# Kernel tuning notes

Measured on AMD Instinct MI355X. Metric: run time of the kernel, lower is better.

## Reference

```python
import jax, jax.numpy as jnp
import numpy as np

FEAT_DIM = 64   # C
EMBED_DIM = 64  # E
NUM_HEADS = 4
B, K, H, W = 4, 8, 128, 128


def setup_inputs() -> dict:
    key = jax.random.key(0)
    ks = jax.random.split(key, 24)
    C, E = FEAT_DIM, EMBED_DIM

    def lin_w(k, out_d, in_d):
        return jax.random.normal(k, (out_d, in_d), jnp.float32) * (1.0 / np.sqrt(in_d))

    def lin_b(k, out_d):
        return jax.random.normal(k, (out_d,), jnp.float32) * 0.01

    return {
        "HF_star": jax.random.normal(ks[0], (B, C, H, W), jnp.float32),
        "HF_cands": jax.random.normal(ks[1], (B, K, C, H, W), jnp.float32),
        "Z_cands": jax.random.normal(ks[2], (B, K, C, H, W), jnp.float32),
        "q1_w": lin_w(ks[3], E, C + 2), "q1_b": lin_b(ks[4], E),
        "k1_w": lin_w(ks[5], E, C + 2), "k1_b": lin_b(ks[6], E),
        "v1_w": lin_w(ks[7], E, C), "v1_b": lin_b(ks[8], E),
        "q2_w": lin_w(ks[9], E, C + E + 2), "q2_b": lin_b(ks[10], E),
        "k2_w": lin_w(ks[11], E, C + E + 2), "k2_b": lin_b(ks[12], E),
        "v2_w": lin_w(ks[13], E, C + E), "v2_b": lin_b(ks[14], E),
        "in_proj_w": lin_w(ks[15], 3 * E, E), "in_proj_b": lin_b(ks[16], 3 * E),
        "out_w": lin_w(ks[17], E, E), "out_b": lin_b(ks[18], E),
    }


def _mha(q, k, v, in_proj_w, in_proj_b, out_w, out_b, num_heads):
    # Replicates torch nn.MultiheadAttention with query len 1 per pixel.
    # q: [BN, E], k/v: [BN, K, E]
    E = q.shape[-1]
    d = E // num_heads
    wq, wk, wv = jnp.split(in_proj_w, 3, axis=0)
    bq, bk, bv = jnp.split(in_proj_b, 3, axis=0)
    qh = (q @ wq.T + bq).reshape(-1, num_heads, d)                  # [BN,h,d]
    kh = (k @ wk.T + bk).reshape(k.shape[0], k.shape[1], num_heads, d)  # [BN,K,h,d]
    vh = (v @ wv.T + bv).reshape(v.shape[0], v.shape[1], num_heads, d)
    scale = 1.0 / np.sqrt(d).astype(np.float32)
    scores = jnp.einsum('bhd,bkhd->bhk', qh, kh) * scale            # [BN,h,K]
    attn = jax.nn.softmax(scores, axis=-1)
    out = jnp.einsum('bhk,bkhd->bhd', attn, vh).reshape(-1, E)      # [BN,E]
    return out @ out_w.T + out_b


def reference(HF_star, HF_cands, Z_cands,
              q1_w, q1_b, k1_w, k1_b, v1_w, v1_b,
              q2_w, q2_b, k2_w, k2_b, v2_w, v2_b,
              in_proj_w, in_proj_b, out_w, out_b):
    Bb, C, Hh, Ww = HF_star.shape
    Kk = HF_cands.shape[1]
    N = Hh * Ww
    E = out_w.shape[0]

    i = jnp.linspace(0.0, 1.0, Hh)
    j = jnp.linspace(0.0, 1.0, Ww)
    ig, jg = jnp.meshgrid(i, j, indexing='ij')
    coords = jnp.stack([ig, jg], axis=-1)                            # [H,W,2]

    Qpix = jnp.transpose(HF_star, (0, 2, 3, 1))                      # [B,H,W,C]
    Kc = jnp.transpose(HF_cands, (0, 1, 3, 4, 2))                    # [B,K,H,W,C]
    Vc = jnp.transpose(Z_cands, (0, 1, 3, 4, 2))                     # [B,K,H,W,C]
    coords_q = jnp.broadcast_to(coords, (Bb, Hh, Ww, 2))
    coords_k = jnp.broadcast_to(coords, (Bb, Kk, Hh, Ww, 2))

    # Stage 1 (note: key reshape [B,K,H,W,D] -> [B*N,K,D] matches torch reshape semantics)
    Q1 = jnp.concatenate([Qpix, coords_q], axis=-1).reshape(Bb * N, C + 2)
    K1 = jnp.concatenate([Kc, coords_k], axis=-1).reshape(Bb * N, Kk, C + 2)
    V1 = Vc.reshape(Bb * N, Kk, C)
    q = Q1 @ q1_w.T + q1_b
    k = K1 @ k1_w.T + k1_b
    v = V1 @ v1_w.T + v1_b
    z_star = _mha(q, k, v, in_proj_w, in_proj_b, out_w, out_b, NUM_HEADS)
    z_bhwe = z_star.reshape(Bb, Hh, Ww, E)                           # [B,H,W,E]
    z_k = jnp.broadcast_to(z_bhwe[:, None], (Bb, Kk, Hh, Ww, E))

    # Stage 2
    Q2 = jnp.concatenate([Qpix, z_bhwe, coords_q], axis=-1).reshape(Bb * N, C + E + 2)
    K2 = jnp.concatenate([Kc, z_k, coords_k], axis=-1).reshape(Bb * N, Kk, C + E + 2)
    V2 = jnp.concatenate([Vc, z_k], axis=-1).reshape(Bb * N, Kk, C + E)
    q = Q2 @ q2_w.T + q2_b
    k = K2 @ k2_w.T + k2_b
    v = V2 @ v2_w.T + v2_b
    z_hat = _mha(q, k, v, in_proj_w, in_proj_b, out_w, out_b, NUM_HEADS)
    return jnp.transpose(z_hat.reshape(Bb, Hh, Ww, E), (0, 3, 1, 2))  # [B,E,H,W]
```

## Files before the change

### kernel.cpp

```cpp
#include <hip/hip_runtime.h>
#include <math.h>

#define HWp 16384
#define CH 64
#define KC 8
#define WSTRIDE 136

typedef __attribute__((ext_vector_type(8))) short bf16x8;
typedef __attribute__((ext_vector_type(4))) float f32x4;

#define MFMA(a, b, c) __builtin_amdgcn_mfma_f32_16x16x32_bf16(a, b, c, 0, 0, 0)

__device__ __forceinline__ short f2bf(float f) {
  unsigned u = __float_as_uint(f);
  u += 0x7FFFu + ((u >> 16) & 1u);
  return (short)(u >> 16);
}
__device__ __forceinline__ float bf2f(short s) {
  return __uint_as_float(((unsigned)(unsigned short)s) << 16);
}

__device__ __forceinline__ bf16x8 ldB(const short* __restrict__ W, int nrow, int c0) {
  return *(const bf16x8*)(W + nrow * WSTRIDE + c0);
}
__device__ __forceinline__ bf16x8 ldA_g(const float* __restrict__ base, int c0, int row) {
  bf16x8 f;
#pragma unroll
  for (int j = 0; j < 8; ++j) f[j] = f2bf(base[(size_t)(c0 + j) * HWp + row]);
  return f;
}
__device__ __forceinline__ bf16x8 ldA_z(const short* __restrict__ zrow, int c0) {
  return *(const bf16x8*)(zrow + c0);
}

__global__ void setup_weights(const float* __restrict__ q1w, const float* __restrict__ q1b,
                              const float* __restrict__ k1w, const float* __restrict__ k1b,
                              const float* __restrict__ v1w, const float* __restrict__ v1b,
                              const float* __restrict__ q2w, const float* __restrict__ q2b,
                              const float* __restrict__ k2w, const float* __restrict__ k2b,
                              const float* __restrict__ v2w, const float* __restrict__ v2b,
                              const float* __restrict__ ipw, const float* __restrict__ ipb,
                              const float* __restrict__ ow, short* __restrict__ Wt,
                              float* __restrict__ Bc) {
  int id = blockIdx.y;
  int idx = blockIdx.x * 256 + threadIdx.x;
  if (id == 6) {
    if (idx < 4096) {
      int e = idx >> 6, d = idx & 63;
      Wt[(6 * 64 + e) * WSTRIDE + d] = f2bf(ow[e * 64 + d]);
    }
    return;
  }
  const float* lw; const float* lb; int K, off;
  switch (id) {
    case 0:  lw = q1w; lb = q1b; K = 66;  off = 0;   break;
    case 1:  lw = k1w; lb = k1b; K = 66;  off = 64;  break;
    case 2:  lw = v1w; lb = v1b; K = 64;  off = 128; break;
    case 3:  lw = q2w; lb = q2b; K = 130; off = 0;   break;
    case 4:  lw = k2w; lb = k2b; K = 130; off = 64;  break;
    default: lw = v2w; lb = v2b; K = 128; off = 128; break;
  }
  if (idx < K * 64) {
    int c = idx >> 6, e = idx & 63;
    float s = 0.f;
    for (int f = 0; f < 64; ++f) s += ipw[(off + e) * 64 + f] * lw[f * K + c];
    Wt[(id * 64 + e) * WSTRIDE + c] = f2bf(s);
  } else if (idx < K * 64 + 64) {
    int e = idx - K * 64;
    float s = ipb[off + e];
    for (int f = 0; f < 64; ++f) s += ipw[(off + e) * 64 + f] * lb[f];
    Bc[id * 64 + e] = s;
  }
}

__global__ __launch_bounds__(256) void stage1(const float* __restrict__ HFs,
                                              const float* __restrict__ HFc,
                                              const float* __restrict__ Zc,
                                              const short* __restrict__ Wt,
                                              const float* __restrict__ Bc,
                                              const float* __restrict__ outb,
                                              short* __restrict__ zb) {
  const int t = threadIdx.x;
  const int wv = t >> 6, l = t & 63;
  const int tile = blockIdx.x;
  const int b = tile >> 11;
  const int p0 = (tile & 2047) << 3;
  const int m0 = p0 << 3;
  const int k0 = m0 >> 14;
  const int poff = m0 & (HWp - 1);

  __shared__ float KV[64 * 77];
  __shared__ float QH[8 * 68];
  __shared__ float AO[8 * 68];
  __shared__ float ATT[256];

  const int am = l & 15, kg = l >> 4, n = l & 15;
  const int row0 = wv * 16;

  const short* Wq = Wt + 0 * 64 * WSTRIDE;
  const short* Wk = Wt + 1 * 64 * WSTRIDE;
  const short* Wv = Wt + 2 * 64 * WSTRIDE;
  const short* Wo = Wt + 6 * 64 * WSTRIDE;
  const float* BQ = Bc + 0 * 64;
  const float* BK = Bc + 1 * 64;
  const float* BV = Bc + 2 * 64;

  const float* baseKc = HFc + ((size_t)(b * KC + k0) * CH) * HWp + poff;
  const float* baseZc = Zc + ((size_t)(b * KC + k0) * CH) * HWp + poff;
  const float* baseQ = HFs + (size_t)b * CH * HWp;
  const float inv127 = 1.f / 127.f;

  f32x4 kacc[4];
#pragma unroll
  for (int ct = 0; ct < 4; ++ct) {
    int col = ct * 16 + n;
    float bk = BK[col];
    float wi = bf2f(Wk[col * WSTRIDE + 64]);
    float wj = bf2f(Wk[col * WSTRIDE + 65]);
#pragma unroll
    for (int r = 0; r < 4; ++r) {
      int pp = poff + row0 + kg * 4 + r;
      kacc[ct][r] = bk + (float)(pp >> 7) * inv127 * wi + (float)(pp & 127) * inv127 * wj;
    }
  }
  f32x4 qacc;
  {
    int colq = wv * 16 + n;
    float bq = BQ[colq];
    float wi = bf2f(Wq[colq * WSTRIDE + 64]);
    float wj = bf2f(Wq[colq * WSTRIDE + 65]);
#pragma unroll
    for (int r = 0; r < 4; ++r) {
      int p = p0 + ((kg * 4 + r) & 7);
      qacc[r] = bq + (float)(p >> 7) * inv127 * wi + (float)(p & 127) * inv127 * wj;
    }
  }
#pragma unroll
  for (int ks = 0; ks < 2; ++ks) {
    int c0 = ks * 32 + kg * 8;
    bf16x8 a = ldA_g(baseKc, c0, row0 + am);
#pragma unroll
    for (int ct = 0; ct < 4; ++ct) kacc[ct] = MFMA(a, ldB(Wk, ct * 16 + n, c0), kacc[ct]);
    bf16x8 aq = ldA_g(baseQ, c0, p0 + (am & 7));
    qacc = MFMA(aq, ldB(Wq, wv * 16 + n, c0), qacc);
  }
#pragma unroll
  for (int ct = 0; ct < 4; ++ct)
#pragma unroll
    for (int r = 0; r < 4; ++r)
      KV[(row0 + kg * 4 + r) * 77 + ct * 16 + n] = kacc[ct][r];
#pragma unroll
  for (int r = 0; r < 4; ++r) {
    int m = kg * 4 + r;
    if (m < 8) QH[m * 68 + wv * 16 + n] = qacc[r];
  }
  __syncthreads();

  {
    int p = t >> 5, k = t & 7, h = (t >> 3) & 3;
    const float* qrow = &QH[p * 68 + h * 16];
    const float* krow = &KV[(p * 8 + k) * 77 + h * 16];
    float s = 0.f;
#pragma unroll
    for (int d = 0; d < 16; ++d) s += qrow[d] * krow[d];
    s *= 0.25f;
    float mx = s;
    mx = fmaxf(mx, __shfl_xor(mx, 1));
    mx = fmaxf(mx, __shfl_xor(mx, 2));
    mx = fmaxf(mx, __shfl_xor(mx, 4));
    float e = __expf(s - mx);
    float sum = e;
    sum += __shfl_xor(sum, 1);
    sum += __shfl_xor(sum, 2);
    sum += __shfl_xor(sum, 4);
    ATT[t] = e / sum;
  }
  __syncthreads();

  f32x4 vacc[4];
#pragma unroll
  for (int ct = 0; ct < 4; ++ct) {
    float bv = BV[ct * 16 + n];
#pragma unroll
    for (int r = 0; r < 4; ++r) vacc[ct][r] = bv;
  }
#pragma unroll
  for (int ks = 0; ks < 2; ++ks) {
    int c0 = ks * 32 + kg * 8;
    bf16x8 a = ldA_g(baseZc, c0, row0 + am);
#pragma unroll
    for (int ct = 0; ct < 4; ++ct) vacc[ct] = MFMA(a, ldB(Wv, ct * 16 + n, c0), vacc[ct]);
  }
#pragma unroll
  for (int ct = 0; ct < 4; ++ct)
#pragma unroll
    for (int r = 0; r < 4; ++r)
      KV[(row0 + kg * 4 + r) * 77 + ct * 16 + n] = vacc[ct][r];
  __syncthreads();

  {
    int p = t >> 5, dp = t & 7, h = (t >> 3) & 3;
    int d0 = h * 16 + dp * 2;
    float o0 = 0.f, o1 = 0.f;
#pragma unroll
    for (int k = 0; k < 8; ++k) {
      float a = ATT[(t & ~7) + k];
      const float* vrow = &KV[(p * 8 + k) * 77 + d0];
      o0 += a * vrow[0];
      o1 += a * vrow[1];
    }
    AO[p * 68 + d0] = o0;
    AO[p * 68 + d0 + 1] = o1;
  }
  __syncthreads();

  {
    int colo = wv * 16 + n;
    f32x4 oacc;
    float bo = outb[colo];
#pragma unroll
    for (int r = 0; r < 4; ++r) oacc[r] = bo;
#pragma unroll
    for (int ks = 0; ks < 2; ++ks) {
      int c0 = ks * 32 + kg * 8;
      bf16x8 a;
#pragma unroll
      for (int j = 0; j < 8; ++j) a[j] = f2bf(AO[(am & 7) * 68 + c0 + j]);
      oacc = MFMA(a, ldB(Wo, colo, c0), oacc);
    }
#pragma unroll
    for (int r = 0; r < 4; ++r) {
      int m = kg * 4 + r;
      if (m < 8) zb[((size_t)(b * HWp + p0 + m)) * 64 + colo] = f2bf(oacc[r]);
    }
  }
}

__global__ __launch_bounds__(256) void stage2(const float* __restrict__ HFs,
                                              const float* __restrict__ HFc,
                                              const float* __restrict__ Zc,
                                              const short* __restrict__ Wt,
                                              const float* __restrict__ Bc,
                                              const float* __restrict__ outb,
                                              const short* __restrict__ zb,
                                              float* __restrict__ out) {
  const int t = threadIdx.x;
  const int wv = t >> 6, l = t & 63;
  const int tile = blockIdx.x;
  const int b = tile >> 11;
  const int p0 = (tile & 2047) << 3;
  const int m0 = p0 << 3;
  const int k0 = m0 >> 14;
  const int poff = m0 & (HWp - 1);

  __shared__ float KV[64 * 77];
  __shared__ float QH[8 * 68];
  __shared__ float AO[8 * 68];
  __shared__ float ATT[256];

  const int am = l & 15, kg = l >> 4, n = l & 15;
  const int row0 = wv * 16;

  const short* Wq = Wt + 3 * 64 * WSTRIDE;
  const short* Wk = Wt + 4 * 64 * WSTRIDE;
  const short* Wv = Wt + 5 * 64 * WSTRIDE;
  const short* Wo = Wt + 6 * 64 * WSTRIDE;
  const float* BQ = Bc + 3 * 64;
  const float* BK = Bc + 4 * 64;
  const float* BV = Bc + 5 * 64;

  const float* baseKc = HFc + ((size_t)(b * KC + k0) * CH) * HWp + poff;
  const float* baseZc = Zc + ((size_t)(b * KC + k0) * CH) * HWp + poff;
  const float* baseQ = HFs + (size_t)b * CH * HWp;
  const short* zK = zb + ((size_t)(b * HWp + poff + row0 + am)) * 64;
  const short* zQ = zb + ((size_t)(b * HWp + p0 + (am & 7))) * 64;
  const float inv127 = 1.f / 127.f;

  f32x4 kacc[4];
#pragma unroll
  for (int ct = 0; ct < 4; ++ct) {
    int col = ct * 16 + n;
    float bk = BK[col];
    float wi = bf2f(Wk[col * WSTRIDE + 128]);
    float wj = bf2f(Wk[col * WSTRIDE + 129]);
#pragma unroll
    for (int r = 0; r < 4; ++r) {
      int pp = poff + row0 + kg * 4 + r;
      kacc[ct][r] = bk + (float)(pp >> 7) * inv127 * wi + (float)(pp & 127) * inv127 * wj;
    }
  }
  f32x4 qacc;
  {
    int colq = wv * 16 + n;
    float bq = BQ[colq];
    float wi = bf2f(Wq[colq * WSTRIDE + 128]);
    float wj = bf2f(Wq[colq * WSTRIDE + 129]);
#pragma unroll
    for (int r = 0; r < 4; ++r) {
      int p = p0 + ((kg * 4 + r) & 7);
      qacc[r] = bq + (float)(p >> 7) * inv127 * wi + (float)(p & 127) * inv127 * wj;
    }
  }
#pragma unroll
  for (int ks = 0; ks < 4; ++ks) {
    int c0 = ks * 32 + kg * 8;
    bf16x8 a = (ks < 2) ? ldA_g(baseKc, c0, row0 + am) : ldA_z(zK, c0 - 64);
#pragma unroll
    for (int ct = 0; ct < 4; ++ct) kacc[ct] = MFMA(a, ldB(Wk, ct * 16 + n, c0), kacc[ct]);
    bf16x8 aq = (ks < 2) ? ldA_g(baseQ, c0, p0 + (am & 7)) : ldA_z(zQ, c0 - 64);
    qacc = MFMA(aq, ldB(Wq, wv * 16 + n, c0), qacc);
  }
#pragma unroll
  for (int ct = 0; ct < 4; ++ct)
#pragma unroll
    for (int r = 0; r < 4; ++r)
      KV[(row0 + kg * 4 + r) * 77 + ct * 16 + n] = kacc[ct][r];
#pragma unroll
  for (int r = 0; r < 4; ++r) {
    int m = kg * 4 + r;
    if (m < 8) QH[m * 68 + wv * 16 + n] = qacc[r];
  }
  __syncthreads();

  {
    int p = t >> 5, k = t & 7, h = (t >> 3) & 3;
    const float* qrow = &QH[p * 68 + h * 16];
    const float* krow = &KV[(p * 8 + k) * 77 + h * 16];
    float s = 0.f;
#pragma unroll
    for (int d = 0; d < 16; ++d) s += qrow[d] * krow[d];
    s *= 0.25f;
    float mx = s;
    mx = fmaxf(mx, __shfl_xor(mx, 1));
    mx = fmaxf(mx, __shfl_xor(mx, 2));
    mx = fmaxf(mx, __shfl_xor(mx, 4));
    float e = __expf(s - mx);
    float sum = e;
    sum += __shfl_xor(sum, 1);
    sum += __shfl_xor(sum, 2);
    sum += __shfl_xor(sum, 4);
    ATT[t] = e / sum;
  }
  __syncthreads();

  f32x4 vacc[4];
#pragma unroll
  for (int ct = 0; ct < 4; ++ct) {
    float bv = BV[ct * 16 + n];
#pragma unroll
    for (int r = 0; r < 4; ++r) vacc[ct][r] = bv;
  }
#pragma unroll
  for (int ks = 0; ks < 4; ++ks) {
    int c0 = ks * 32 + kg * 8;
    bf16x8 a = (ks < 2) ? ldA_g(baseZc, c0, row0 + am) : ldA_z(zK, c0 - 64);
#pragma unroll
    for (int ct = 0; ct < 4; ++ct) vacc[ct] = MFMA(a, ldB(Wv, ct * 16 + n, c0), vacc[ct]);
  }
#pragma unroll
  for (int ct = 0; ct < 4; ++ct)
#pragma unroll
    for (int r = 0; r < 4; ++r)
      KV[(row0 + kg * 4 + r) * 77 + ct * 16 + n] = vacc[ct][r];
  __syncthreads();

  {
    int p = t >> 5, dp = t & 7, h = (t >> 3) & 3;
    int d0 = h * 16 + dp * 2;
    float o0 = 0.f, o1 = 0.f;
#pragma unroll
    for (int k = 0; k < 8; ++k) {
      float a = ATT[(t & ~7) + k];
      const float* vrow = &KV[(p * 8 + k) * 77 + d0];
      o0 += a * vrow[0];
      o1 += a * vrow[1];
    }
    AO[p * 68 + d0] = o0;
    AO[p * 68 + d0 + 1] = o1;
  }
  __syncthreads();

  {
    int colo = wv * 16 + n;
    f32x4 oacc;
    float bo = outb[colo];
#pragma unroll
    for (int r = 0; r < 4; ++r) oacc[r] = bo;
#pragma unroll
    for (int ks = 0; ks < 2; ++ks) {
      int c0 = ks * 32 + kg * 8;
      bf16x8 a;
#pragma unroll
      for (int j = 0; j < 8; ++j) a[j] = f2bf(AO[(am & 7) * 68 + c0 + j]);
      oacc = MFMA(a, ldB(Wo, colo, c0), oacc);
    }
#pragma unroll
    for (int r = 0; r < 4; ++r) {
      int m = kg * 4 + r;
      if (m < 8) out[((size_t)(b * 64 + colo)) * HWp + p0 + m] = oacc[r];
    }
  }
}

extern "C" void kernel_launch(void* const* d_in, const int* in_sizes, int n_in,
                              void* d_out, int out_size, void* d_ws, size_t ws_size,
                              hipStream_t stream) {
  const float* HFs = (const float*)d_in[0];
  const float* HFc = (const float*)d_in[1];
  const float* Zc = (const float*)d_in[2];
  const float* q1w = (const float*)d_in[3];  const float* q1b = (const float*)d_in[4];
  const float* k1w = (const float*)d_in[5];  const float* k1b = (const float*)d_in[6];
  const float* v1w = (const float*)d_in[7];  const float* v1b = (const float*)d_in[8];
  const float* q2w = (const float*)d_in[9];  const float* q2b = (const float*)d_in[10];
  const float* k2w = (const float*)d_in[11]; const float* k2b = (const float*)d_in[12];
  const float* v2w = (const float*)d_in[13]; const float* v2b = (const float*)d_in[14];
  const float* ipw = (const float*)d_in[15]; const float* ipb = (const float*)d_in[16];
  const float* ow = (const float*)d_in[17];  const float* ob = (const float*)d_in[18];

  short* Wt = (short*)d_ws;
  float* Bc = (float*)((char*)d_ws + 121856);
  short* zb = (short*)((char*)d_ws + 131072);
  float* out = (float*)d_out;

  dim3 gsetup(33, 7);
  setup_weights<<<gsetup, 256, 0, stream>>>(q1w, q1b, k1w, k1b, v1w, v1b,
                                            q2w, q2b, k2w, k2b, v2w, v2b,
                                            ipw, ipb, ow, Wt, Bc);
  stage1<<<8192, 256, 0, stream>>>(HFs, HFc, Zc, Wt, Bc, ob, zb);
  stage2<<<8192, 256, 0, stream>>>(HFs, HFc, Zc, Wt, Bc, ob, zb, out);
}
```

Baseline: 542.7 us.

## Stage channel-major activation tiles into swizzled LDS with vectorized loads

Replaces per-lane scalar strided global loads (8 channels at HWp stride each) for the K, V and Q MFMA operands with a cooperative up-front staging step. Each thread issues float4 loads along the pixel dimension, converts to bf16, and writes into XOR-swizzled shared tiles. MFMA A-operands are then read as 16-byte LDS vectors. This aims to coalesce global traffic and cut redundant uncoalesced loads, at the cost of roughly 17KB extra LDS per block (lower occupancy) and an added barrier. V loads are now issued early, before attention, which also overlaps them.

```diff
diff --git a/kernel.cpp b/kernel.cpp
--- a/kernel.cpp
+++ b/kernel.cpp
@@ -23,14 +23,44 @@
 __device__ __forceinline__ bf16x8 ldB(const short* __restrict__ W, int nrow, int c0) {
   return *(const bf16x8*)(W + nrow * WSTRIDE + c0);
 }
-__device__ __forceinline__ bf16x8 ldA_g(const float* __restrict__ base, int c0, int row) {
-  bf16x8 f;
-#pragma unroll
-  for (int j = 0; j < 8; ++j) f[j] = f2bf(base[(size_t)(c0 + j) * HWp + row]);
-  return f;
-}
 __device__ __forceinline__ bf16x8 ldA_z(const short* __restrict__ zrow, int c0) {
   return *(const bf16x8*)(zrow + c0);
+}
+
+__device__ __forceinline__ bf16x8 ldT(const short* tile, int p, int c0) {
+  return *(const bf16x8*)(tile + p * 64 + ((((c0 >> 3) ^ p) & 7) << 3));
+}
+
+__device__ __forceinline__ void stage_tile(short* dst, const float* __restrict__ src, int t) {
+  const int ch = (t >> 3) << 1;
+  const int pg = (t & 7) << 3;
+  const float* r0 = src + (size_t)ch * HWp + pg;
+  const float* r1 = r0 + HWp;
+  f32x4 a0 = *(const f32x4*)r0;
+  f32x4 a1 = *(const f32x4*)(r0 + 4);
+  f32x4 b0 = *(const f32x4*)r1;
+  f32x4 b1 = *(const f32x4*)(r1 + 4);
+  const int cb = (ch >> 3) & 7;
+  const int cs = ch & 7;
+#pragma unroll
+  for (int j = 0; j < 8; ++j) {
+    float fa = (j < 4) ? a0[j & 3] : a1[j & 3];
+    float fb = (j < 4) ? b0[j & 3] : b1[j & 3];
+    unsigned dw = (unsigned)(unsigned short)f2bf(fa) |
+                  ((unsigned)(unsigned short)f2bf(fb) << 16);
+    *(unsigned*)(dst + (pg + j) * 64 + ((cb ^ j) << 3) + cs) = dw;
+  }
+}
+
+__device__ __forceinline__ void stage_q(short* dst, const float* __restrict__ src, int t) {
+  const int c = t >> 2;
+  const int p2 = (t & 3) << 1;
+  float x0 = src[(size_t)c * HWp + p2];
+  float x1 = src[(size_t)c * HWp + p2 + 1];
+  const int cb = (c >> 3) & 7;
+  const int cs = c & 7;
+  dst[p2 * 64 + ((cb ^ (p2 & 7)) << 3) + cs] = f2bf(x0);
+  dst[(p2 + 1) * 64 + ((cb ^ ((p2 + 1) & 7)) << 3) + cs] = f2bf(x1);
 }
 
 __global__ void setup_weights(const float* __restrict__ q1w, const float* __restrict__ q1b,
@@ -93,6 +123,9 @@
   __shared__ float QH[8 * 68];
   __shared__ float AO[8 * 68];
   __shared__ float ATT[256];
+  __shared__ __align__(16) short KT[64 * 64];
+  __shared__ __align__(16) short VT[64 * 64];
+  __shared__ __align__(16) short QT[8 * 64];
 
   const int am = l & 15, kg = l >> 4, n = l & 15;
   const int row0 = wv * 16;
@@ -110,6 +143,10 @@
   const float* baseQ = HFs + (size_t)b * CH * HWp;
   const float inv127 = 1.f / 127.f;
 
+  stage_tile(KT, baseKc, t);
+  stage_tile(VT, baseZc, t);
+  stage_q(QT, baseQ + p0, t);
+
   f32x4 kacc[4];
 #pragma unroll
   for (int ct = 0; ct < 4; ++ct) {
@@ -135,13 +172,14 @@
       qacc[r] = bq + (float)(p >> 7) * inv127 * wi + (float)(p & 127) * inv127 * wj;
     }
   }
+  __syncthreads();
 #pragma unroll
   for (int ks = 0; ks < 2; ++ks) {
     int c0 = ks * 32 + kg * 8;
-    bf16x8 a = ldA_g(baseKc, c0, row0 + am);
+    bf16x8 a = ldT(KT, row0 + am, c0);
 #pragma unroll
     for (int ct = 0; ct < 4; ++ct) kacc[ct] = MFMA(a, ldB(Wk, ct * 16 + n, c0), kacc[ct]);
-    bf16x8 aq = ldA_g(baseQ, c0, p0 + (am & 7));
+    bf16x8 aq = ldT(QT, am & 7, c0);
     qacc = MFMA(aq, ldB(Wq, wv * 16 + n, c0), qacc);
   }
 #pragma unroll
@@ -187,7 +225,7 @@
 #pragma unroll
   for (int ks = 0; ks < 2; ++ks) {
     int c0 = ks * 32 + kg * 8;
-    bf16x8 a = ldA_g(baseZc, c0, row0 + am);
+    bf16x8 a = ldT(VT, row0 + am, c0);
 #pragma unroll
     for (int ct = 0; ct < 4; ++ct) vacc[ct] = MFMA(a, ldB(Wv, ct * 16 + n, c0), vacc[ct]);
   }
@@ -257,6 +295,9 @@
   __shared__ float QH[8 * 68];
   __shared__ float AO[8 * 68];
   __shared__ float ATT[256];
+  __shared__ __align__(16) short KT[64 * 64];
+  __shared__ __align__(16) short VT[64 * 64];
+  __shared__ __align__(16) short QT[8 * 64];
 
   const int am = l & 15, kg = l >> 4, n = l & 15;
   const int row0 = wv * 16;
@@ -276,6 +317,10 @@
   const short* zQ = zb + ((size_t)(b * HWp + p0 + (am & 7))) * 64;
   const float inv127 = 1.f / 127.f;
 
+  stage_tile(KT, baseKc, t);
+  stage_tile(VT, baseZc, t);
+  stage_q(QT, baseQ + p0, t);
+
   f32x4 kacc[4];
 #pragma unroll
   for (int ct = 0; ct < 4; ++ct) {
@@ -301,13 +346,14 @@
       qacc[r] = bq + (float)(p >> 7) * inv127 * wi + (float)(p & 127) * inv127 * wj;
     }
   }
+  __syncthreads();
 #pragma unroll
   for (int ks = 0; ks < 4; ++ks) {
     int c0 = ks * 32 + kg * 8;
-    bf16x8 a = (ks < 2) ? ldA_g(baseKc, c0, row0 + am) : ldA_z(zK, c0 - 64);
+    bf16x8 a = (ks < 2) ? ldT(KT, row0 + am, c0) : ldA_z(zK, c0 - 64);
 #pragma unroll
     for (int ct = 0; ct < 4; ++ct) kacc[ct] = MFMA(a, ldB(Wk, ct * 16 + n, c0), kacc[ct]);
-    bf16x8 aq = (ks < 2) ? ldA_g(baseQ, c0, p0 + (am & 7)) : ldA_z(zQ, c0 - 64);
+    bf16x8 aq = (ks < 2) ? ldT(QT, am & 7, c0) : ldA_z(zQ, c0 - 64);
     qacc = MFMA(aq, ldB(Wq, wv * 16 + n, c0), qacc);
   }
 #pragma unroll
@@ -353,7 +399,7 @@
 #pragma unroll
   for (int ks = 0; ks < 4; ++ks) {
     int c0 = ks * 32 + kg * 8;
-    bf16x8 a = (ks < 2) ? ldA_g(baseZc, c0, row0 + am) : ldA_z(zK, c0 - 64);
+    bf16x8 a = (ks < 2) ? ldT(VT, row0 + am, c0) : ldA_z(zK, c0 - 64);
 #pragma unroll
     for (int ct = 0; ct < 4; ++ct) vacc[ct] = MFMA(a, ldB(Wv, ct * 16 + n, c0), vacc[ct]);
   }
```

After: 495.7 us. 8.7% less time.

## Stage coalesced bf16 input tiles in swizzled LDS with register prefetch across 4 tiles

Applied to the files above, without the earlier changes.

Each block now processes four 8-pixel tiles instead of one, cutting the grid from 8192 to 2048 blocks. Input candidate and query features are loaded with vectorized float4 coalesced reads into registers, converted to bf16, and written into XOR-swizzled LDS tiles. The next tile's loads are double-buffered in registers so global latency overlaps compute. This replaces the old strided scalar per-element global gathers, at the cost of more LDS and registers, which may lower occupancy.

```diff
diff --git a/kernel.cpp b/kernel.cpp
--- a/kernel.cpp
+++ b/kernel.cpp
@@ -5,6 +5,7 @@
 #define CH 64
 #define KC 8
 #define WSTRIDE 136
+#define NT 4
 
 typedef __attribute__((ext_vector_type(8))) short bf16x8;
 typedef __attribute__((ext_vector_type(4))) float f32x4;
@@ -23,14 +24,56 @@
 __device__ __forceinline__ bf16x8 ldB(const short* __restrict__ W, int nrow, int c0) {
   return *(const bf16x8*)(W + nrow * WSTRIDE + c0);
 }
-__device__ __forceinline__ bf16x8 ldA_g(const float* __restrict__ base, int c0, int row) {
-  bf16x8 f;
-#pragma unroll
-  for (int j = 0; j < 8; ++j) f[j] = f2bf(base[(size_t)(c0 + j) * HWp + row]);
-  return f;
-}
-__device__ __forceinline__ bf16x8 ldA_z(const short* __restrict__ zrow, int c0) {
-  return *(const bf16x8*)(zrow + c0);
+
+__device__ __forceinline__ bf16x8 ldT(const short* tile, int p, int c0) {
+  return *(const bf16x8*)(tile + p * 64 + ((((c0 >> 3) ^ p) & 7) << 3));
+}
+
+struct Stage {
+  f32x4 k[4];
+  f32x4 v[4];
+  float q0, q1;
+};
+
+__device__ __forceinline__ void ld_rows(f32x4 v[4], const float* __restrict__ src, int t) {
+  const int chg = t >> 4, pxg = t & 15;
+  const float* r = src + (size_t)(chg << 2) * HWp + (pxg << 2);
+#pragma unroll
+  for (int i = 0; i < 4; ++i) v[i] = *(const f32x4*)(r + (size_t)i * HWp);
+}
+
+__device__ __forceinline__ void ld_stage(Stage& s, const float* __restrict__ bK,
+                                         const float* __restrict__ bV,
+                                         const float* __restrict__ bQ, int t) {
+  ld_rows(s.k, bK, t);
+  ld_rows(s.v, bV, t);
+  const int c = t >> 2, p2 = (t & 3) << 1;
+  s.q0 = bQ[(size_t)c * HWp + p2];
+  s.q1 = bQ[(size_t)c * HWp + p2 + 1];
+}
+
+__device__ __forceinline__ void wr_rows(short* dst, const f32x4 v[4], int t) {
+  const int chg = t >> 4, pxg = t & 15;
+  const int ch4 = chg << 2;
+  const int cb = (ch4 >> 3) & 7;
+  const int sub = (ch4 & 7) >> 1;
+#pragma unroll
+  for (int jj = 0; jj < 4; ++jj) {
+    int p = (pxg << 2) + jj;
+    unsigned d0 = (unsigned)(unsigned short)f2bf(v[0][jj]) |
+                  ((unsigned)(unsigned short)f2bf(v[1][jj]) << 16);
+    unsigned d1 = (unsigned)(unsigned short)f2bf(v[2][jj]) |
+                  ((unsigned)(unsigned short)f2bf(v[3][jj]) << 16);
+    unsigned* q = (unsigned*)dst + p * 32 + (((cb ^ (p & 7)) & 7) << 2) + sub;
+    *(uint2*)q = make_uint2(d0, d1);
+  }
+}
+
+__device__ __forceinline__ void wr_q(short* dst, float q0, float q1, int t) {
+  const int c = t >> 2, p2 = (t & 3) << 1;
+  const int cb = (c >> 3) & 7, cs = c & 7;
+  dst[p2 * 64 + (((cb ^ p2) & 7) << 3) + cs] = f2bf(q0);
+  dst[(p2 + 1) * 64 + (((cb ^ (p2 + 1)) & 7) << 3) + cs] = f2bf(q1);
 }
 
 __global__ void setup_weights(const float* __restrict__ q1w, const float* __restrict__ q1b,
@@ -82,17 +125,21 @@
                                               short* __restrict__ zb) {
   const int t = threadIdx.x;
   const int wv = t >> 6, l = t & 63;
-  const int tile = blockIdx.x;
-  const int b = tile >> 11;
-  const int p0 = (tile & 2047) << 3;
-  const int m0 = p0 << 3;
-  const int k0 = m0 >> 14;
-  const int poff = m0 & (HWp - 1);
+  const int bid = blockIdx.x;
+  const int b = bid >> 9;
+  const int pt0 = (bid & 511) << 2;
+  const int p0b = pt0 << 3;
+  const int m0b = p0b << 3;
+  const int k0 = m0b >> 14;
+  const int poffb = m0b & (HWp - 1);
 
   __shared__ float KV[64 * 77];
   __shared__ float QH[8 * 68];
   __shared__ float AO[8 * 68];
   __shared__ float ATT[256];
+  __shared__ __align__(16) short KT[64 * 64];
+  __shared__ __align__(16) short VT[64 * 64];
+  __shared__ __align__(16) short QT[8 * 64];
 
   const int am = l & 15, kg = l >> 4, n = l & 15;
   const int row0 = wv * 16;
@@ -105,134 +152,159 @@
   const float* BK = Bc + 1 * 64;
   const float* BV = Bc + 2 * 64;
 
-  const float* baseKc = HFc + ((size_t)(b * KC + k0) * CH) * HWp + poff;
-  const float* baseZc = Zc + ((size_t)(b * KC + k0) * CH) * HWp + poff;
+  const float* baseKc = HFc + ((size_t)(b * KC + k0) * CH) * HWp + poffb;
+  const float* baseZc = Zc + ((size_t)(b * KC + k0) * CH) * HWp + poffb;
   const float* baseQ = HFs + (size_t)b * CH * HWp;
   const float inv127 = 1.f / 127.f;
 
-  f32x4 kacc[4];
-#pragma unroll
-  for (int ct = 0; ct < 4; ++ct) {
-    int col = ct * 16 + n;
-    float bk = BK[col];
-    float wi = bf2f(Wk[col * WSTRIDE + 64]);
-    float wj = bf2f(Wk[col * WSTRIDE + 65]);
-#pragma unroll
-    for (int r = 0; r < 4; ++r) {
-      int pp = poff + row0 + kg * 4 + r;
-      kacc[ct][r] = bk + (float)(pp >> 7) * inv127 * wi + (float)(pp & 127) * inv127 * wj;
-    }
-  }
-  f32x4 qacc;
-  {
-    int colq = wv * 16 + n;
-    float bq = BQ[colq];
-    float wi = bf2f(Wq[colq * WSTRIDE + 64]);
-    float wj = bf2f(Wq[colq * WSTRIDE + 65]);
-#pragma unroll
-    for (int r = 0; r < 4; ++r) {
-      int p = p0 + ((kg * 4 + r) & 7);
-      qacc[r] = bq + (float)(p >> 7) * inv127 * wi + (float)(p & 127) * inv127 * wj;
-    }
-  }
-#pragma unroll
-  for (int ks = 0; ks < 2; ++ks) {
-    int c0 = ks * 32 + kg * 8;
-    bf16x8 a = ldA_g(baseKc, c0, row0 + am);
-#pragma unroll
-    for (int ct = 0; ct < 4; ++ct) kacc[ct] = MFMA(a, ldB(Wk, ct * 16 + n, c0), kacc[ct]);
-    bf16x8 aq = ldA_g(baseQ, c0, p0 + (am & 7));
-    qacc = MFMA(aq, ldB(Wq, wv * 16 + n, c0), qacc);
-  }
-#pragma unroll
-  for (int ct = 0; ct < 4; ++ct)
-#pragma unroll
-    for (int r = 0; r < 4; ++r)
-      KV[(row0 + kg * 4 + r) * 77 + ct * 16 + n] = kacc[ct][r];
-#pragma unroll
-  for (int r = 0; r < 4; ++r) {
-    int m = kg * 4 + r;
-    if (m < 8) QH[m * 68 + wv * 16 + n] = qacc[r];
-  }
+  Stage st[2];
+  ld_stage(st[0], baseKc, baseZc, baseQ + p0b, t);
+  ld_stage(st[1], baseKc + 64, baseZc + 64, baseQ + p0b + 8, t);
+  wr_rows(KT, st[0].k, t);
+  wr_rows(VT, st[0].v, t);
+  wr_q(QT, st[0].q0, st[0].q1, t);
   __syncthreads();
 
-  {
-    int p = t >> 5, k = t & 7, h = (t >> 3) & 3;
-    const float* qrow = &QH[p * 68 + h * 16];
-    const float* krow = &KV[(p * 8 + k) * 77 + h * 16];
-    float s = 0.f;
-#pragma unroll
-    for (int d = 0; d < 16; ++d) s += qrow[d] * krow[d];
-    s *= 0.25f;
-    float mx = s;
-    mx = fmaxf(mx, __shfl_xor(mx, 1));
-    mx = fmaxf(mx, __shfl_xor(mx, 2));
-    mx = fmaxf(mx, __shfl_xor(mx, 4));
-    float e = __expf(s - mx);
-    float sum = e;
-    sum += __shfl_xor(sum, 1);
-    sum += __shfl_xor(sum, 2);
-    sum += __shfl_xor(sum, 4);
-    ATT[t] = e / sum;
-  }
-  __syncthreads();
-
-  f32x4 vacc[4];
-#pragma unroll
-  for (int ct = 0; ct < 4; ++ct) {
-    float bv = BV[ct * 16 + n];
-#pragma unroll
-    for (int r = 0; r < 4; ++r) vacc[ct][r] = bv;
-  }
-#pragma unroll
-  for (int ks = 0; ks < 2; ++ks) {
-    int c0 = ks * 32 + kg * 8;
-    bf16x8 a = ldA_g(baseZc, c0, row0 + am);
-#pragma unroll
-    for (int ct = 0; ct < 4; ++ct) vacc[ct] = MFMA(a, ldB(Wv, ct * 16 + n, c0), vacc[ct]);
-  }
-#pragma unroll
-  for (int ct = 0; ct < 4; ++ct)
-#pragma unroll
-    for (int r = 0; r < 4; ++r)
-      KV[(row0 + kg * 4 + r) * 77 + ct * 16 + n] = vacc[ct][r];
-  __syncthreads();
-
-  {
-    int p = t >> 5, dp = t & 7, h = (t >> 3) & 3;
-    int d0 = h * 16 + dp * 2;
-    float o0 = 0.f, o1 = 0.f;
-#pragma unroll
-    for (int k = 0; k < 8; ++k) {
-      float a = ATT[(t & ~7) + k];
-      const float* vrow = &KV[(p * 8 + k) * 77 + d0];
-      o0 += a * vrow[0];
-      o1 += a * vrow[1];
-    }
-    AO[p * 68 + d0] = o0;
-    AO[p * 68 + d0 + 1] = o1;
-  }
-  __syncthreads();
-
-  {
-    int colo = wv * 16 + n;
-    f32x4 oacc;
-    float bo = outb[colo];
-#pragma unroll
-    for (int r = 0; r < 4; ++r) oacc[r] = bo;
+#pragma unroll
+  for (int j = 0; j < NT; ++j) {
+    const int p0 = p0b + j * 8;
+    const int poff = poffb + j * 64;
+
+    f32x4 kacc[4];
+#pragma unroll
+    for (int ct = 0; ct < 4; ++ct) {
+      int col = ct * 16 + n;
+      float bk = BK[col];
+      float wi = bf2f(Wk[col * WSTRIDE + 64]);
+      float wj = bf2f(Wk[col * WSTRIDE + 65]);
+#pragma unroll
+      for (int r = 0; r < 4; ++r) {
+        int pp = poff + row0 + kg * 4 + r;
+        kacc[ct][r] = bk + (float)(pp >> 7) * inv127 * wi + (float)(pp & 127) * inv127 * wj;
+      }
+    }
+    f32x4 qacc;
+    {
+      int colq = wv * 16 + n;
+      float bq = BQ[colq];
+      float wi = bf2f(Wq[colq * WSTRIDE + 64]);
+      float wj = bf2f(Wq[colq * WSTRIDE + 65]);
+#pragma unroll
+      for (int r = 0; r < 4; ++r) {
+        int p = p0 + ((kg * 4 + r) & 7);
+        qacc[r] = bq + (float)(p >> 7) * inv127 * wi + (float)(p & 127) * inv127 * wj;
+      }
+    }
 #pragma unroll
     for (int ks = 0; ks < 2; ++ks) {
       int c0 = ks * 32 + kg * 8;
-      bf16x8 a;
-#pragma unroll
-      for (int j = 0; j < 8; ++j) a[j] = f2bf(AO[(am & 7) * 68 + c0 + j]);
-      oacc = MFMA(a, ldB(Wo, colo, c0), oacc);
-    }
+      bf16x8 a = ldT(KT, row0 + am, c0);
+#pragma unroll
+      for (int ct = 0; ct < 4; ++ct) kacc[ct] = MFMA(a, ldB(Wk, ct * 16 + n, c0), kacc[ct]);
+      bf16x8 aq = ldT(QT, am & 7, c0);
+      qacc = MFMA(aq, ldB(Wq, wv * 16 + n, c0), qacc);
+    }
+#pragma unroll
+    for (int ct = 0; ct < 4; ++ct)
+#pragma unroll
+      for (int r = 0; r < 4; ++r)
+        KV[(row0 + kg * 4 + r) * 77 + ct * 16 + n] = kacc[ct][r];
 #pragma unroll
     for (int r = 0; r < 4; ++r) {
       int m = kg * 4 + r;
-      if (m < 8) zb[((size_t)(b * HWp + p0 + m)) * 64 + colo] = f2bf(oacc[r]);
-    }
+      if (m < 8) QH[m * 68 + wv * 16 + n] = qacc[r];
+    }
+    __syncthreads();
+
+    {
+      int p = t >> 5, k = t & 7, h = (t >> 3) & 3;
+      const float* qrow = &QH[p * 68 + h * 16];
+      const float* krow = &KV[(p * 8 + k) * 77 + h * 16];
+      float s = 0.f;
+#pragma unroll
+      for (int d = 0; d < 16; ++d) s += qrow[d] * krow[d];
+      s *= 0.25f;
+      float mx = s;
+      mx = fmaxf(mx, __shfl_xor(mx, 1));
+      mx = fmaxf(mx, __shfl_xor(mx, 2));
+      mx = fmaxf(mx, __shfl_xor(mx, 4));
+      float e = __expf(s - mx);
+      float sum = e;
+      sum += __shfl_xor(sum, 1);
+      sum += __shfl_xor(sum, 2);
+      sum += __shfl_xor(sum, 4);
+      ATT[t] = e / sum;
+    }
+    __syncthreads();
+
+    f32x4 vacc[4];
+#pragma unroll
+    for (int ct = 0; ct < 4; ++ct) {
+      float bv = BV[ct * 16 + n];
+#pragma unroll
+      for (int r = 0; r < 4; ++r) vacc[ct][r] = bv;
+    }
+#pragma unroll
+    for (int ks = 0; ks < 2; ++ks) {
+      int c0 = ks * 32 + kg * 8;
+      bf16x8 a = ldT(VT, row0 + am, c0);
+#pragma unroll
+      for (int ct = 0; ct < 4; ++ct) vacc[ct] = MFMA(a, ldB(Wv, ct * 16 + n, c0), vacc[ct]);
+    }
+#pragma unroll
+    for (int ct = 0; ct < 4; ++ct)
+#pragma unroll
+      for (int r = 0; r < 4; ++r)
+        KV[(row0 + kg * 4 + r) * 77 + ct * 16 + n] = vacc[ct][r];
+    __syncthreads();
+
+    {
+      int p = t >> 5, dp = t & 7, h = (t >> 3) & 3;
+      int d0 = h * 16 + dp * 2;
+      float o0 = 0.f, o1 = 0.f;
+#pragma unroll
+      for (int k = 0; k < 8; ++k) {
+        float a = ATT[(t & ~7) + k];
+        const float* vrow = &KV[(p * 8 + k) * 77 + d0];
+        o0 += a * vrow[0];
+        o1 += a * vrow[1];
+      }
+      AO[p * 68 + d0] = o0;
+      AO[p * 68 + d0 + 1] = o1;
+    }
+    __syncthreads();
+
+    {
+      int colo = wv * 16 + n;
+      f32x4 oacc;
+      float bo = outb[colo];
+#pragma unroll
+      for (int r = 0; r < 4; ++r) oacc[r] = bo;
+#pragma unroll
+      for (int ks = 0; ks < 2; ++ks) {
+        int c0 = ks * 32 + kg * 8;
+        bf16x8 a;
+#pragma unroll
+        for (int q = 0; q < 8; ++q) a[q] = f2bf(AO[(am & 7) * 68 + c0 + q]);
+        oacc = MFMA(a, ldB(Wo, colo, c0), oacc);
+      }
+#pragma unroll
+      for (int r = 0; r < 4; ++r) {
+        int m = kg * 4 + r;
+        if (m < 8) zb[((size_t)(b * HWp + p0 + m)) * 64 + colo] = f2bf(oacc[r]);
+      }
+    }
+
+    if (j < NT - 1) {
+      Stage& nx = st[(j + 1) & 1];
+      wr_rows(KT, nx.k, t);
+      wr_rows(VT, nx.v, t);
+      wr_q(QT, nx.q0, nx.q1, t);
+      if (j < NT - 2)
+        ld_stage(st[j & 1], baseKc + (j + 2) * 64, baseZc + (j + 2) * 64,
+                 baseQ + p0b + (j + 2) * 8, t);
+    }
+    __syncthreads();
   }
 }
 
@@ -246,17 +318,21 @@
                                               float* __restrict__ out) {
   const int t = threadIdx.x;
   const int wv = t >> 6, l = t & 63;
-  const int tile = blockIdx.x;
-  const int b = tile >> 11;
-  const int p0 = (tile & 2047) << 3;
-  const int m0 = p0 << 3;
-  const int k0 = m0 >> 14;
-  const int poff = m0 & (HWp - 1);
+  const int bid = blockIdx.x;
+  const int b = bid >> 9;
+  const int pt0 = (bid & 511) << 2;
+  const int p0b = pt0 << 3;
+  const int m0b = p0b << 3;
+  const int k0 = m0b >> 14;
+  const int poffb = m0b & (HWp - 1);
 
   __shared__ float KV[64 * 77];
   __shared__ float QH[8 * 68];
   __shared__ float AO[8 * 68];
   __shared__ float ATT[256];
+  __shared__ __align__(16) short KT[64 * 64];
+  __shared__ __align__(16) short VT[64 * 64];
+  __shared__ __align__(16) short QT[8 * 64];
 
   const int am = l & 15, kg = l >> 4, n = l & 15;
   const int row0 = wv * 16;
@@ -269,136 +345,166 @@
   const float* BK = Bc + 4 * 64;
   const float* BV = Bc + 5 * 64;
 
-  const float* baseKc = HFc + ((size_t)(b * KC + k0) * CH) * HWp + poff;
-  const float* baseZc = Zc + ((size_t)(b * KC + k0) * CH) * HWp + poff;
+  const float* baseKc = HFc + ((size_t)(b * KC + k0) * CH) * HWp + poffb;
+  const float* baseZc = Zc + ((size_t)(b * KC + k0) * CH) * HWp + poffb;
   const float* baseQ = HFs + (size_t)b * CH * HWp;
-  const short* zK = zb + ((size_t)(b * HWp + poff + row0 + am)) * 64;
-  const short* zQ = zb + ((size_t)(b * HWp + p0 + (am & 7))) * 64;
   const float inv127 = 1.f / 127.f;
 
-  f32x4 kacc[4];
-#pragma unroll
-  for (int ct = 0; ct < 4; ++ct) {
-    int col = ct * 16 + n;
-    float bk = BK[col];
-    float wi = bf2f(Wk[col * WSTRIDE + 128]);
-    float wj = bf2f(Wk[col * WSTRIDE + 129]);
-#pragma unroll
-    for (int r = 0; r < 4; ++r) {
-      int pp = poff + row0 + kg * 4 + r;
-      kacc[ct][r] = bk + (float)(pp >> 7) * inv127 * wi + (float)(pp & 127) * inv127 * wj;
-    }
-  }
-  f32x4 qacc;
-  {
-    int colq = wv * 16 + n;
-    float bq = BQ[colq];
-    float wi = bf2f(Wq[colq * WSTRIDE + 128]);
-    float wj = bf2f(Wq[colq * WSTRIDE + 129]);
-#pragma unroll
-    for (int r = 0; r < 4; ++r) {
-      int p = p0 + ((kg * 4 + r) & 7);
-      qacc[r] = bq + (float)(p >> 7) * inv127 * wi + (float)(p & 127) * inv127 * wj;
-    }
-  }
-#pragma unroll
-  for (int ks = 0; ks < 4; ++ks) {
-    int c0 = ks * 32 + kg * 8;
-    bf16x8 a = (ks < 2) ? ldA_g(baseKc, c0, row0 + am) : ldA_z(zK, c0 - 64);
-#pragma unroll
-    for (int ct = 0; ct < 4; ++ct) kacc[ct] = MFMA(a, ldB(Wk, ct * 16 + n, c0), kacc[ct]);
-    bf16x8 aq = (ks < 2) ? ldA_g(baseQ, c0, p0 + (am & 7)) : ldA_z(zQ, c0 - 64);
-    qacc = MFMA(aq, ldB(Wq, wv * 16 + n, c0), qacc);
-  }
-#pragma unroll
-  for (int ct = 0; ct < 4; ++ct)
-#pragma unroll
-    for (int r = 0; r < 4; ++r)
-      KV[(row0 + kg * 4 + r) * 77 + ct * 16 + n] = kacc[ct][r];
-#pragma unroll
-  for (int r = 0; r < 4; ++r) {
-    int m = kg * 4 + r;
-    if (m < 8) QH[m * 68 + wv * 16 + n] = qacc[r];
-  }
+  Stage st[2];
+  ld_stage(st[0], baseKc, baseZc, baseQ + p0b, t);
+  ld_stage(st[1], baseKc + 64, baseZc + 64, baseQ + p0b + 8, t);
+  wr_rows(KT, st[0].k, t);
+  wr_rows(VT, st[0].v, t);
+  wr_q(QT, st[0].q0, st[0].q1, t);
   __syncthreads();
 
-  {
-    int p = t >> 5, k = t & 7, h = (t >> 3) & 3;
-    const float* qrow = &QH[p * 68 + h * 16];
-    const float* krow = &KV[(p * 8 + k) * 77 + h * 16];
-    float s = 0.f;
-#pragma unroll
-    for (int d = 0; d < 16; ++d) s += qrow[d] * krow[d];
-    s *= 0.25f;
-    float mx = s;
-    mx = fmaxf(mx, __shfl_xor(mx, 1));
-    mx = fmaxf(mx, __shfl_xor(mx, 2));
-    mx = fmaxf(mx, __shfl_xor(mx, 4));
-    float e = __expf(s - mx);
-    float sum = e;
-    sum += __shfl_xor(sum, 1);
-    sum += __shfl_xor(sum, 2);
-    sum += __shfl_xor(sum, 4);
-    ATT[t] = e / sum;
-  }
-  __syncthreads();
-
-  f32x4 vacc[4];
-#pragma unroll
-  for (int ct = 0; ct < 4; ++ct) {
-    float bv = BV[ct * 16 + n];
-#pragma unroll
-    for (int r = 0; r < 4; ++r) vacc[ct][r] = bv;
-  }
-#pragma unroll
-  for (int ks = 0; ks < 4; ++ks) {
-    int c0 = ks * 32 + kg * 8;
-    bf16x8 a = (ks < 2) ? ldA_g(baseZc, c0, row0 + am) : ldA_z(zK, c0 - 64);
-#pragma unroll
-    for (int ct = 0; ct < 4; ++ct) vacc[ct] = MFMA(a, ldB(Wv, ct * 16 + n, c0), vacc[ct]);
-  }
-#pragma unroll
-  for (int ct = 0; ct < 4; ++ct)
-#pragma unroll
-    for (int r = 0; r < 4; ++r)
-      KV[(row0 + kg * 4 + r) * 77 + ct * 16 + n] = vacc[ct][r];
-  __syncthreads();
-
-  {
-    int p = t >> 5, dp = t & 7, h = (t >> 3) & 3;
-    int d0 = h * 16 + dp * 2;
-    float o0 = 0.f, o1 = 0.f;
-#pragma unroll
-    for (int k = 0; k < 8; ++k) {
-      float a = ATT[(t & ~7) + k];
-      const float* vrow = &KV[(p * 8 + k) * 77 + d0];
-      o0 += a * vrow[0];
-      o1 += a * vrow[1];
-    }
-    AO[p * 68 + d0] = o0;
-    AO[p * 68 + d0 + 1] = o1;
-  }
-  __syncthreads();
-
-  {
-    int colo = wv * 16 + n;
-    f32x4 oacc;
-    float bo = outb[colo];
-#pragma unroll
-    for (int r = 0; r < 4; ++r) oacc[r] = bo;
-#pragma unroll
-    for (int ks = 0; ks < 2; ++ks) {
+#pragma unroll
+  for (int j = 0; j < NT; ++j) {
+    const int p0 = p0b + j * 8;
+    const int poff = poffb + j * 64;
+
+    const short* zKr = zb + ((size_t)(b * HWp + poff + row0 + am)) * 64 + kg * 8;
+    bf16x8 zk0 = *(const bf16x8*)zKr;
+    bf16x8 zk1 = *(const bf16x8*)(zKr + 32);
+    const short* zQr = zb + ((size_t)(b * HWp + p0 + (am & 7))) * 64 + kg * 8;
+    bf16x8 zq0 = *(const bf16x8*)zQr;
+    bf16x8 zq1 = *(const bf16x8*)(zQr + 32);
+
+    f32x4 kacc[4];
+#pragma unroll
+    for (int ct = 0; ct < 4; ++ct) {
+      int col = ct * 16 + n;
+      float bk = BK[col];
+      float wi = bf2f(Wk[col * WSTRIDE + 128]);
+      float wj = bf2f(Wk[col * WSTRIDE + 129]);
+#pragma unroll
+      for (int r = 0; r < 4; ++r) {
+        int pp = poff + row0 + kg * 4 + r;
+        kacc[ct][r] = bk + (float)(pp >> 7) * inv127 * wi + (float)(pp & 127) * inv127 * wj;
+      }
+    }
+    f32x4 qacc;
+    {
+      int colq = wv * 16 + n;
+      float bq = BQ[colq];
+      float wi = bf2f(Wq[colq * WSTRIDE + 128]);
+      float wj = bf2f(Wq[colq * WSTRIDE + 129]);
+#pragma unroll
+      for (int r = 0; r < 4; ++r) {
+        int p = p0 + ((kg * 4 + r) & 7);
+        qacc[r] = bq + (float)(p >> 7) * inv127 * wi + (float)(p & 127) * inv127 * wj;
+      }
+    }
+#pragma unroll
+    for (int ks = 0; ks < 4; ++ks) {
       int c0 = ks * 32 + kg * 8;
-      bf16x8 a;
-#pragma unroll
-      for (int j = 0; j < 8; ++j) a[j] = f2bf(AO[(am & 7) * 68 + c0 + j]);
-      oacc = MFMA(a, ldB(Wo, colo, c0), oacc);
-    }
+      bf16x8 a = (ks < 2) ? ldT(KT, row0 + am, c0) : (ks == 2 ? zk0 : zk1);
+#pragma unroll
+      for (int ct = 0; ct < 4; ++ct) kacc[ct] = MFMA(a, ldB(Wk, ct * 16 + n, c0), kacc[ct]);
+      bf16x8 aq = (ks < 2) ? ldT(QT, am & 7, c0) : (ks == 2 ? zq0 : zq1);
+      qacc = MFMA(aq, ldB(Wq, wv * 16 + n, c0), qacc);
+    }
+#pragma unroll
+    for (int ct = 0; ct < 4; ++ct)
+#pragma unroll
+      for (int r = 0; r < 4; ++r)
+        KV[(row0 + kg * 4 + r) * 77 + ct * 16 + n] = kacc[ct][r];
 #pragma unroll
     for (int r = 0; r < 4; ++r) {
       int m = kg * 4 + r;
-      if (m < 8) out[((size_t)(b * 64 + colo)) * HWp + p0 + m] = oacc[r];
-    }
+      if (m < 8) QH[m * 68 + wv * 16 + n] = qacc[r];
+    }
+    __syncthreads();
+
+    {
+      int p = t >> 5, k = t & 7, h = (t >> 3) & 3;
+      const float* qrow = &QH[p * 68 + h * 16];
+      const float* krow = &KV[(p * 8 + k) * 77 + h * 16];
+      float s = 0.f;
+#pragma unroll
+      for (int d = 0; d < 16; ++d) s += qrow[d] * krow[d];
+      s *= 0.25f;
+      float mx = s;
+      mx = fmaxf(mx, __shfl_xor(mx, 1));
+      mx = fmaxf(mx, __shfl_xor(mx, 2));
+      mx = fmaxf(mx, __shfl_xor(mx, 4));
+      float e = __expf(s - mx);
+      float sum = e;
+      sum += __shfl_xor(sum, 1);
+      sum += __shfl_xor(sum, 2);
+      sum += __shfl_xor(sum, 4);
+      ATT[t] = e / sum;
+    }
+    __syncthreads();
+
+    f32x4 vacc[4];
+#pragma unroll
+    for (int ct = 0; ct < 4; ++ct) {
+      float bv = BV[ct * 16 + n];
+#pragma unroll
+      for (int r = 0; r < 4; ++r) vacc[ct][r] = bv;
+    }
+#pragma unroll
+    for (int ks = 0; ks < 4; ++ks) {
+      int c0 = ks * 32 + kg * 8;
+      bf16x8 a = (ks < 2) ? ldT(VT, row0 + am, c0) : (ks == 2 ? zk0 : zk1);
+#pragma unroll
+      for (int ct = 0; ct < 4; ++ct) vacc[ct] = MFMA(a, ldB(Wv, ct * 16 + n, c0), vacc[ct]);
+    }
+#pragma unroll
+    for (int ct = 0; ct < 4; ++ct)
+#pragma unroll
+      for (int r = 0; r < 4; ++r)
+        KV[(row0 + kg * 4 + r) * 77 + ct * 16 + n] = vacc[ct][r];
+    __syncthreads();
+
+    {
+      int p = t >> 5, dp = t & 7, h = (t >> 3) & 3;
+      int d0 = h * 16 + dp * 2;
+      float o0 = 0.f, o1 = 0.f;
+#pragma unroll
+      for (int k = 0; k < 8; ++k) {
+        float a = ATT[(t & ~7) + k];
+        const float* vrow = &KV[(p * 8 + k) * 77 + d0];
+        o0 += a * vrow[0];
+        o1 += a * vrow[1];
+      }
+      AO[p * 68 + d0] = o0;
+      AO[p * 68 + d0 + 1] = o1;
+    }
+    __syncthreads();
+
+    {
+      int colo = wv * 16 + n;
+      f32x4 oacc;
+      float bo = outb[colo];
+#pragma unroll
+      for (int r = 0; r < 4; ++r) oacc[r] = bo;
+#pragma unroll
+      for (int ks = 0; ks < 2; ++ks) {
+        int c0 = ks * 32 + kg * 8;
+        bf16x8 a;
+#pragma unroll
+        for (int q = 0; q < 8; ++q) a[q] = f2bf(AO[(am & 7) * 68 + c0 + q]);
+        oacc = MFMA(a, ldB(Wo, colo, c0), oacc);
+      }
+#pragma unroll
+      for (int r = 0; r < 4; ++r) {
+        int m = kg * 4 + r;
+        if (m < 8) out[((size_t)(b * 64 + colo)) * HWp + p0 + m] = oacc[r];
+      }
+    }
+
+    if (j < NT - 1) {
+      Stage& nx = st[(j + 1) & 1];
+      wr_rows(KT, nx.k, t);
+      wr_rows(VT, nx.v, t);
+      wr_q(QT, nx.q0, nx.q1, t);
+      if (j < NT - 2)
+        ld_stage(st[j & 1], baseKc + (j + 2) * 64, baseZc + (j + 2) * 64,
+                 baseQ + p0b + (j + 2) * 8, t);
+    }
+    __syncthreads();
   }
 }
 
@@ -426,6 +532,6 @@
   setup_weights<<<gsetup, 256, 0, stream>>>(q1w, q1b, k1w, k1b, v1w, v1b,
                                             q2w, q2b, k2w, k2b, v2w, v2b,
                                             ipw, ipb, ow, Wt, Bc);
-  stage1<<<8192, 256, 0, stream>>>(HFs, HFc, Zc, Wt, Bc, ob, zb);
-  stage2<<<8192, 256, 0, stream>>>(HFs, HFc, Zc, Wt, Bc, ob, zb, out);
-}
+  stage1<<<2048, 256, 0, stream>>>(HFs, HFc, Zc, Wt, Bc, ob, zb);
+  stage2<<<2048, 256, 0, stream>>>(HFs, HFc, Zc, Wt, Bc, ob, zb, out);
+}
```

Result: faster. 508.1 us (-6.4%).
